# Optimization experiments

Measured on AMD Instinct MI355X. Metric: run time of the kernel, lower is better.

The kernel has to match this reference:

```python
import jax, jax.numpy as jnp
import numpy as np

CODEBOOK_SIZE = 1024
CODEBOOK_DIM = 10  # log2(1024)
CODEBOOK_SCALE = 1.0
ENTROPY_W = 1.0
COMMIT_W = 1.0
DIVERSITY_GAMMA = 1.0
INV_TEMPERATURE = 100.0


def _wn_conv1x1(x_bdt, v, g, b):
    # weight_norm over (in, k) per out channel; kernel_size=1 -> plain matmul
    w = g[:, None] * v / jnp.linalg.norm(v, axis=1, keepdims=True)  # [out, in]
    return jnp.einsum('oi,bit->bot', w, x_bdt) + b[None, :, None]


def _make_codebook():
    codes = jnp.arange(CODEBOOK_SIZE)
    shifts = jnp.arange(CODEBOOK_DIM - 1, -1, -1)
    bits = ((codes[:, None] >> shifts[None, :]) & 1).astype(jnp.float32)
    return bits * 2.0 * CODEBOOK_SCALE - CODEBOOK_SCALE  # [cs, cd]


def setup_inputs() -> dict:
    key = jax.random.key(0)
    ks = jax.random.split(key, 7)
    B, D, T = 16, 512, 4096
    cd = CODEBOOK_DIM
    return {
        'x': jax.random.normal(ks[0], (B, D, T), dtype=jnp.float32),
        'in_v': jax.random.normal(ks[1], (cd, D), dtype=jnp.float32),
        'in_g': jax.random.uniform(ks[2], (cd,), dtype=jnp.float32) + 0.5,
        'in_b': jax.random.normal(ks[3], (cd,), dtype=jnp.float32) * 0.01,
        'out_v': jax.random.normal(ks[4], (D, cd), dtype=jnp.float32),
        'out_g': jax.random.uniform(ks[5], (D,), dtype=jnp.float32) + 0.5,
        'out_b': jax.random.normal(ks[6], (D,), dtype=jnp.float32) * 0.01,
    }


def reference(x, in_v, in_g, in_b, out_v, out_g, out_b):
    codebook = _make_codebook()                       # [cs, cd]
    mask = (2 ** jnp.arange(CODEBOOK_DIM - 1, -1, -1)).astype(jnp.int32)

    xp = _wn_conv1x1(x, in_v, in_g, in_b)             # [b, cd, t]
    orig = jnp.transpose(xp, (0, 2, 1))               # [b, t, cd]

    quantized = jnp.where(orig > 0, CODEBOOK_SCALE, -CODEBOOK_SCALE).astype(orig.dtype)
    indices = jnp.sum((quantized > 0).astype(jnp.int32) * mask, axis=-1)  # [b, t]

    # straight-through estimator (training mode)
    q_ste = orig + jax.lax.stop_gradient(quantized - orig)

    # distance = -2 * orig @ codebook^T; prob = softmax(-distance * inv_temp)
    logits = (2.0 * INV_TEMPERATURE) * jnp.einsum('btd,jd->btj', orig, codebook)
    prob = jax.nn.softmax(logits, axis=-1)            # [b, t, cs]

    per_sample_entropy = jnp.mean(
        jnp.sum(-prob * jnp.log(jnp.clip(prob, 1e-5)), axis=-1))
    avg_prob = jnp.mean(prob, axis=(0, 1))            # [cs]
    codebook_entropy = jnp.sum(-avg_prob * jnp.log(jnp.clip(avg_prob, 1e-5)))
    entropy_aux_loss = per_sample_entropy - DIVERSITY_GAMMA * codebook_entropy

    commit_loss = jnp.mean((orig - jax.lax.stop_gradient(quantized)) ** 2)

    out = _wn_conv1x1(jnp.transpose(q_ste, (0, 2, 1)), out_v, out_g, out_b)  # [b, D, t]
    aux_loss = entropy_aux_loss * ENTROPY_W + commit_loss * COMMIT_W
    return out, indices, aux_loss
```

## Files before the change

### kernel.cpp

```cpp
#include <hip/hip_runtime.h>
#include <math.h>

#define B_   16
#define D_   512
#define T_   4096
#define CD   10
#define CS   1024
#define NTOK (B_*T_)
#define TPB_A 128
#define NBLK_A (NTOK/TPB_A)

typedef float f32x2 __attribute__((ext_vector_type(2)));
typedef float f32x4 __attribute__((ext_vector_type(4)));

#define WS_WT     0
#define WS_PARTH  5120
#define WS_PARTC  6144
#define WS_HIST   7168
#define WS_HMID   531456

__global__ __launch_bounds__(256) void prep_wt(
    const float* __restrict__ in_v, const float* __restrict__ in_g,
    float* __restrict__ w_t)
{
  __shared__ double pn[16];
  __shared__ float nrm_s;
  const int d   = blockIdx.x;
  const int tid = threadIdx.x;
  if (tid < 16) {
    double s = 0.0;
    const float* vp = in_v + d*D_ + tid*32;
    #pragma unroll
    for (int k = 0; k < 32; ++k) { double v = (double)vp[k]; s += v*v; }
    pn[tid] = s;
  }
  __syncthreads();
  if (tid == 0) {
    double s = 0.0;
    #pragma unroll
    for (int j = 0; j < 16; ++j) s += pn[j];
    nrm_s = (float)sqrt(s);
  }
  __syncthreads();
  const float g = in_g[d], nrm = nrm_s;
  for (int D = tid; D < D_; D += 256)
    w_t[D*CD + d] = g * in_v[d*D_ + D] / nrm;
}

__global__ __launch_bounds__(256) void lfq_fused(
    const float* __restrict__ x, const float* __restrict__ in_b,
    const float* __restrict__ w_t,
    const float* __restrict__ out_v, const float* __restrict__ out_g,
    const float* __restrict__ out_b,
    float* __restrict__ out, float* __restrict__ out_idx,
    float* __restrict__ partH, float* __restrict__ partC,
    float* __restrict__ hist_part)
{
  __shared__ float  hist[CS];
  __shared__ int    sidx[TPB_A];
  __shared__ double red[4*TPB_A*CD];
  __shared__ float  wn[D_*CD];
  __shared__ float  ob[D_];

  const int tid  = threadIdx.x;
  const int blk  = blockIdx.x;
  const int b    = blk >> 5;
  const int t0   = (blk & 31) * TPB_A;
  const int wave = __builtin_amdgcn_readfirstlane(tid >> 6);
  const int lane = tid & 63;

  for (int i = tid; i < CS; i += 256) hist[i] = 0.f;

  double acc[2*CD];
  #pragma unroll
  for (int i = 0; i < 2*CD; ++i) acc[i] = 0.0;
  const float* xb = x + ((size_t)b * D_ + wave * 128) * T_ + t0 + 2*lane;
  const float* wp = w_t + (size_t)wave * 128 * CD;
  #pragma unroll 8
  for (int Di = 0; Di < 128; ++Di) {
    f32x2 xv = __builtin_nontemporal_load(
                    (const f32x2*)(xb + (size_t)Di * T_));
    double x0 = (double)xv.x, x1 = (double)xv.y;
    const f32x2* w2 = (const f32x2*)(wp + Di * CD);
    #pragma unroll
    for (int i = 0; i < 5; ++i) {
      f32x2 w = w2[i];
      acc[4*i+0] += (double)w.x * x0;
      acc[4*i+1] += (double)w.x * x1;
      acc[4*i+2] += (double)w.y * x0;
      acc[4*i+3] += (double)w.y * x1;
    }
  }
  #pragma unroll
  for (int d = 0; d < CD; ++d) {
    red[((size_t)wave*TPB_A + 2*lane + 0)*CD + d] = acc[2*d+0];
    red[((size_t)wave*TPB_A + 2*lane + 1)*CD + d] = acc[2*d+1];
  }
  __syncthreads();

  if (wave < 2) {
    const int ti = wave*64 + lane;
    float Hs = 0.f, C = 0.f;
    int   idx = 0;
    int   k = 0; int pos[CD]; float ms[CD];
    #pragma unroll
    for (int d = 0; d < CD; ++d) {
      double o = red[(size_t)(0*TPB_A + ti)*CD + d]
               + red[(size_t)(1*TPB_A + ti)*CD + d]
               + red[(size_t)(2*TPB_A + ti)*CD + d]
               + red[(size_t)(3*TPB_A + ti)*CD + d]
               + (double)in_b[d];
      float v = (float)o;
      int bit = (v > 0.f);
      idx |= bit << (9 - d);
      float c = v - (bit ? 1.f : -1.f);
      C += c * c;
      float e = __expf(-400.f * fabsf(v));
      if (e > 1e-9f) { ms[k] = e / (1.f + e); pos[k] = 9 - d; ++k; }
    }
    int nc = 1 << k;
    for (int c = 0; c < nc; ++c) {
      float p = 1.f; int bin = idx;
      for (int i = 0; i < k; ++i) {
        if ((c >> i) & 1) { p *= ms[i]; bin ^= (1 << pos[i]); }
        else              { p *= (1.f - ms[i]); }
      }
      Hs -= p * __logf(fmaxf(p, 1e-5f));
      atomicAdd(&hist[bin], p);
    }
    out_idx[b * T_ + t0 + ti] = (float)idx;
    sidx[ti] = idx;
    #pragma unroll
    for (int off = 32; off > 0; off >>= 1) {
      Hs += __shfl_down(Hs, off, 64);
      C  += __shfl_down(C,  off, 64);
    }
    if (lane == 0) { partH[blk*2 + wave] = Hs; partC[blk*2 + wave] = C; }
  } else {
    const int local = tid - 128;
    #pragma unroll
    for (int r = 0; r < 4; ++r) {
      const int D = local*4 + r;
      const float* vr = out_v + D*CD;
      float vv[CD];
      float s2 = 0.f;
      #pragma unroll
      for (int d = 0; d < CD; ++d) { vv[d] = vr[d]; s2 += vv[d]*vv[d]; }
      const float sc = out_g[D] / sqrtf(s2);
      #pragma unroll
      for (int d = 0; d < CD; ++d) wn[D*CD + d] = vv[d] * sc;
      ob[D] = out_b[D];
    }
  }
  __syncthreads();

  for (int i = tid; i < CS; i += 256) hist_part[(size_t)blk*CS + i] = hist[i];

  const int t4 = (tid & 31) * 4;
  const int c0 = sidx[t4+0], c1 = sidx[t4+1], c2 = sidx[t4+2], c3 = sidx[t4+3];
  const int Dbase = tid >> 5;
  float* op = out + ((size_t)b * D_) * T_ + t0 + t4;
  #pragma unroll 4
  for (int it = 0; it < 64; ++it) {
    const int D = Dbase + it*8;
    const float* wr = wn + D*CD;
    const float base = ob[D];
    float s0 = base, s1 = base, s2 = base, s3 = base;
    #pragma unroll
    for (int d = 0; d < CD; ++d) {
      const float w = wr[d];
      const int sh = 9 - d;
      s0 += ((c0 >> sh) & 1) ? w : -w;
      s1 += ((c1 >> sh) & 1) ? w : -w;
      s2 += ((c2 >> sh) & 1) ? w : -w;
      s3 += ((c3 >> sh) & 1) ? w : -w;
    }
    f32x4 o; o.x = s0; o.y = s1; o.z = s2; o.w = s3;
    __builtin_nontemporal_store(o, (f32x4*)(op + (size_t)D * T_));
  }
}

__global__ __launch_bounds__(256) void hist_reduce(
    const float* __restrict__ hist_part, float* __restrict__ hmid)
{
  int r  = blockIdx.x >> 2;
  int bg = blockIdx.x & 3;
  int bin = bg * 256 + threadIdx.x;
  float s = 0.f;
  for (int m = 0; m < 16; ++m) s += hist_part[(size_t)(r*16 + m)*CS + bin];
  hmid[r*CS + bin] = s;
}

__global__ __launch_bounds__(256) void finalize(
    const float* __restrict__ hmid, const float* __restrict__ partH,
    const float* __restrict__ partC, float* __restrict__ aux_out)
{
  int tid = threadIdx.x;
  float ce = 0.f, h = 0.f, cm = 0.f;
  for (int q = 0; q < 4; ++q) {
    int bin = q*256 + tid;
    float s = 0.f;
    for (int r = 0; r < 32; ++r) s += hmid[r*CS + bin];
    float ap = s * (1.f/65536.f);
    ce += -ap * __logf(fmaxf(ap, 1e-5f));
  }
  for (int i = tid; i < 1024; i += 256) { h += partH[i]; cm += partC[i]; }
  __shared__ float rb[3][256];
  rb[0][tid] = ce; rb[1][tid] = h; rb[2][tid] = cm;
  __syncthreads();
  for (int s = 128; s > 0; s >>= 1) {
    if (tid < s) {
      rb[0][tid] += rb[0][tid+s];
      rb[1][tid] += rb[1][tid+s];
      rb[2][tid] += rb[2][tid+s];
    }
    __syncthreads();
  }
  if (tid == 0) {
    float psH    = rb[1][0] * (1.f/65536.f);
    float commit = rb[2][0] * (1.f/655360.f);
    aux_out[0] = psH - rb[0][0] + commit;
  }
}

extern "C" void kernel_launch(void* const* d_in, const int* in_sizes, int n_in,
                              void* d_out, int out_size, void* d_ws, size_t ws_size,
                              hipStream_t stream) {
  const float* x     = (const float*)d_in[0];
  const float* in_v  = (const float*)d_in[1];
  const float* in_g  = (const float*)d_in[2];
  const float* in_b  = (const float*)d_in[3];
  const float* out_v = (const float*)d_in[4];
  const float* out_g = (const float*)d_in[5];
  const float* out_b = (const float*)d_in[6];

  float* out     = (float*)d_out;
  float* out_idx = out + (size_t)B_*D_*T_;
  float* aux     = out_idx + NTOK;

  float* wsf = (float*)d_ws;

  prep_wt<<<dim3(CD), dim3(256), 0, stream>>>(in_v, in_g, wsf + WS_WT);
  lfq_fused<<<dim3(NBLK_A), dim3(256), 0, stream>>>(
      x, in_b, wsf + WS_WT, out_v, out_g, out_b,
      out, out_idx,
      wsf + WS_PARTH, wsf + WS_PARTC, wsf + WS_HIST);
  hist_reduce<<<dim3(128), dim3(256), 0, stream>>>(wsf + WS_HIST, wsf + WS_HMID);
  finalize<<<dim3(1), dim3(256), 0, stream>>>(wsf + WS_HMID, wsf + WS_PARTH,
                                              wsf + WS_PARTC, aux);
}
```

Baseline: 64.83 us.

## Merge histogram reduce and finalize, spread out-weight prep across all threads

Folds the hist_reduce and finalize kernels into one kernel that uses a last-block ticket counter, cutting one launch. The counter is reset in prep_wt. The output-projection weight normalization now runs on all 256 threads, with out_v loads issued before the main x loop so their latency overlaps it, instead of running only on waves 2-3 after the reduction. Also raises the x loop unroll to 16, vectorizes the histogram and shared-memory weight reads, and uses nontemporal stores for indices and histogram partials. The reduce kernel drops from 128 to 32 blocks, so it has less parallelism, and the higher unroll adds register pressure.

```diff
diff --git a/kernel.cpp b/kernel.cpp
--- a/kernel.cpp
+++ b/kernel.cpp
@@ -16,17 +16,19 @@
 #define WS_WT     0
 #define WS_PARTH  5120
 #define WS_PARTC  6144
-#define WS_HIST   7168
-#define WS_HMID   531456
+#define WS_CNT    7168
+#define WS_HIST   7424
+#define WS_HMID   531712
 
 __global__ __launch_bounds__(256) void prep_wt(
     const float* __restrict__ in_v, const float* __restrict__ in_g,
-    float* __restrict__ w_t)
+    float* __restrict__ w_t, int* __restrict__ counter)
 {
   __shared__ double pn[16];
   __shared__ float nrm_s;
   const int d   = blockIdx.x;
   const int tid = threadIdx.x;
+  if (d == 0 && tid == 0) *counter = 0;
   if (tid < 16) {
     double s = 0.0;
     const float* vp = in_v + d*D_ + tid*32;
@@ -71,12 +73,27 @@
 
   for (int i = tid; i < CS; i += 256) hist[i] = 0.f;
 
+  float vv0[CD], vv1[CD];
+  const int Ds0 = 2*tid, Ds1 = 2*tid + 1;
+  {
+    const f32x2* r0 = (const f32x2*)(out_v + Ds0*CD);
+    const f32x2* r1 = (const f32x2*)(out_v + Ds1*CD);
+    #pragma unroll
+    for (int i = 0; i < 5; ++i) {
+      f32x2 a = r0[i], c = r1[i];
+      vv0[2*i] = a.x; vv0[2*i+1] = a.y;
+      vv1[2*i] = c.x; vv1[2*i+1] = c.y;
+    }
+  }
+  const float g0 = out_g[Ds0], g1 = out_g[Ds1];
+  const float ob0 = out_b[Ds0], ob1 = out_b[Ds1];
+
   double acc[2*CD];
   #pragma unroll
   for (int i = 0; i < 2*CD; ++i) acc[i] = 0.0;
   const float* xb = x + ((size_t)b * D_ + wave * 128) * T_ + t0 + 2*lane;
   const float* wp = w_t + (size_t)wave * 128 * CD;
-  #pragma unroll 8
+  #pragma unroll 16
   for (int Di = 0; Di < 128; ++Di) {
     f32x2 xv = __builtin_nontemporal_load(
                     (const f32x2*)(xb + (size_t)Di * T_));
@@ -95,6 +112,18 @@
   for (int d = 0; d < CD; ++d) {
     red[((size_t)wave*TPB_A + 2*lane + 0)*CD + d] = acc[2*d+0];
     red[((size_t)wave*TPB_A + 2*lane + 1)*CD + d] = acc[2*d+1];
+  }
+  {
+    float s20 = 0.f, s21 = 0.f;
+    #pragma unroll
+    for (int d = 0; d < CD; ++d) { s20 += vv0[d]*vv0[d]; s21 += vv1[d]*vv1[d]; }
+    const float sc0 = g0 / sqrtf(s20), sc1 = g1 / sqrtf(s21);
+    #pragma unroll
+    for (int d = 0; d < CD; ++d) {
+      wn[Ds0*CD + d] = vv0[d] * sc0;
+      wn[Ds1*CD + d] = vv1[d] * sc1;
+    }
+    ob[Ds0] = ob0; ob[Ds1] = ob1;
   }
   __syncthreads();
 
@@ -128,7 +157,7 @@
       Hs -= p * __logf(fmaxf(p, 1e-5f));
       atomicAdd(&hist[bin], p);
     }
-    out_idx[b * T_ + t0 + ti] = (float)idx;
+    __builtin_nontemporal_store((float)idx, out_idx + b * T_ + t0 + ti);
     sidx[ti] = idx;
     #pragma unroll
     for (int off = 32; off > 0; off >>= 1) {
@@ -136,25 +165,13 @@
       C  += __shfl_down(C,  off, 64);
     }
     if (lane == 0) { partH[blk*2 + wave] = Hs; partC[blk*2 + wave] = C; }
-  } else {
-    const int local = tid - 128;
-    #pragma unroll
-    for (int r = 0; r < 4; ++r) {
-      const int D = local*4 + r;
-      const float* vr = out_v + D*CD;
-      float vv[CD];
-      float s2 = 0.f;
-      #pragma unroll
-      for (int d = 0; d < CD; ++d) { vv[d] = vr[d]; s2 += vv[d]*vv[d]; }
-      const float sc = out_g[D] / sqrtf(s2);
-      #pragma unroll
-      for (int d = 0; d < CD; ++d) wn[D*CD + d] = vv[d] * sc;
-      ob[D] = out_b[D];
-    }
-  }
-  __syncthreads();
-
-  for (int i = tid; i < CS; i += 256) hist_part[(size_t)blk*CS + i] = hist[i];
+  }
+  __syncthreads();
+
+  {
+    f32x4 hv = *(const f32x4*)(hist + tid*4);
+    __builtin_nontemporal_store(hv, (f32x4*)(hist_part + (size_t)blk*CS + tid*4));
+  }
 
   const int t4 = (tid & 31) * 4;
   const int c0 = sidx[t4+0], c1 = sidx[t4+1], c2 = sidx[t4+2], c3 = sidx[t4+3];
@@ -163,44 +180,60 @@
   #pragma unroll 4
   for (int it = 0; it < 64; ++it) {
     const int D = Dbase + it*8;
-    const float* wr = wn + D*CD;
+    const f32x2* wr2 = (const f32x2*)(wn + D*CD);
     const float base = ob[D];
     float s0 = base, s1 = base, s2 = base, s3 = base;
     #pragma unroll
-    for (int d = 0; d < CD; ++d) {
-      const float w = wr[d];
-      const int sh = 9 - d;
-      s0 += ((c0 >> sh) & 1) ? w : -w;
-      s1 += ((c1 >> sh) & 1) ? w : -w;
-      s2 += ((c2 >> sh) & 1) ? w : -w;
-      s3 += ((c3 >> sh) & 1) ? w : -w;
+    for (int i = 0; i < 5; ++i) {
+      f32x2 w2v = wr2[i];
+      {
+        const float w = w2v.x; const int sh = 9 - 2*i;
+        s0 += ((c0 >> sh) & 1) ? w : -w;
+        s1 += ((c1 >> sh) & 1) ? w : -w;
+        s2 += ((c2 >> sh) & 1) ? w : -w;
+        s3 += ((c3 >> sh) & 1) ? w : -w;
+      }
+      {
+        const float w = w2v.y; const int sh = 9 - (2*i+1);
+        s0 += ((c0 >> sh) & 1) ? w : -w;
+        s1 += ((c1 >> sh) & 1) ? w : -w;
+        s2 += ((c2 >> sh) & 1) ? w : -w;
+        s3 += ((c3 >> sh) & 1) ? w : -w;
+      }
     }
     f32x4 o; o.x = s0; o.y = s1; o.z = s2; o.w = s3;
     __builtin_nontemporal_store(o, (f32x4*)(op + (size_t)D * T_));
   }
 }
 
-__global__ __launch_bounds__(256) void hist_reduce(
-    const float* __restrict__ hist_part, float* __restrict__ hmid)
+__global__ __launch_bounds__(256) void hist_final(
+    const float* __restrict__ hist_part, const float* __restrict__ partH,
+    const float* __restrict__ partC, float* __restrict__ hmid,
+    int* __restrict__ counter, float* __restrict__ aux_out)
 {
-  int r  = blockIdx.x >> 2;
-  int bg = blockIdx.x & 3;
-  int bin = bg * 256 + threadIdx.x;
-  float s = 0.f;
-  for (int m = 0; m < 16; ++m) s += hist_part[(size_t)(r*16 + m)*CS + bin];
-  hmid[r*CS + bin] = s;
-}
-
-__global__ __launch_bounds__(256) void finalize(
-    const float* __restrict__ hmid, const float* __restrict__ partH,
-    const float* __restrict__ partC, float* __restrict__ aux_out)
-{
-  int tid = threadIdx.x;
+  const int r   = blockIdx.x;
+  const int tid = threadIdx.x;
+  #pragma unroll
+  for (int q = 0; q < 4; ++q) {
+    const int bin = q*256 + tid;
+    float s = 0.f;
+    for (int m = 0; m < 16; ++m)
+      s += hist_part[(size_t)(r*16 + m)*CS + bin];
+    hmid[r*CS + bin] = s;
+  }
+  __threadfence();
+  __shared__ int ticket_s;
+  if (tid == 0) ticket_s = atomicAdd(counter, 1);
+  __syncthreads();
+  if (ticket_s != 31) return;
+  __threadfence();
+
   float ce = 0.f, h = 0.f, cm = 0.f;
+  #pragma unroll
   for (int q = 0; q < 4; ++q) {
-    int bin = q*256 + tid;
+    const int bin = q*256 + tid;
     float s = 0.f;
-    for (int r = 0; r < 32; ++r) s += hmid[r*CS + bin];
+    for (int rr = 0; rr < 32; ++rr) s += hmid[rr*CS + bin];
     float ap = s * (1.f/65536.f);
     ce += -ap * __logf(fmaxf(ap, 1e-5f));
   }
@@ -239,13 +272,14 @@
   float* aux     = out_idx + NTOK;
 
   float* wsf = (float*)d_ws;
-
-  prep_wt<<<dim3(CD), dim3(256), 0, stream>>>(in_v, in_g, wsf + WS_WT);
+  int*   cnt = (int*)(wsf + WS_CNT);
+
+  prep_wt<<<dim3(CD), dim3(256), 0, stream>>>(in_v, in_g, wsf + WS_WT, cnt);
   lfq_fused<<<dim3(NBLK_A), dim3(256), 0, stream>>>(
       x, in_b, wsf + WS_WT, out_v, out_g, out_b,
       out, out_idx,
       wsf + WS_PARTH, wsf + WS_PARTC, wsf + WS_HIST);
-  hist_reduce<<<dim3(128), dim3(256), 0, stream>>>(wsf + WS_HIST, wsf + WS_HMID);
-  finalize<<<dim3(1), dim3(256), 0, stream>>>(wsf + WS_HMID, wsf + WS_PARTH,
-                                              wsf + WS_PARTC, aux);
-}
+  hist_final<<<dim3(32), dim3(256), 0, stream>>>(
+      wsf + WS_HIST, wsf + WS_PARTH, wsf + WS_PARTC,
+      wsf + WS_HMID, cnt, aux);
+}
```

After: 115.2 us. +77.7%, slower.
